# Optimization experiments

Measured on AMD Instinct MI355X. Metric: run time of the kernel, lower is better.

The kernel has to match this reference:

```python
import math
import jax, jax.numpy as jnp
import numpy as np

D_MODEL = 1024
N_HEADS = 16


def setup_inputs() -> dict:
    key = jax.random.key(0)
    ks = jax.random.split(key, 5)
    B, S, D = 4, 2048, D_MODEL
    std = math.sqrt(2.0 / (D + D))
    x = jax.random.normal(ks[0], (B, S, D), dtype=jnp.float32)
    wq = jax.random.normal(ks[1], (D, D), dtype=jnp.float32) * std
    wk = jax.random.normal(ks[2], (D, D), dtype=jnp.float32) * std
    wv = jax.random.normal(ks[3], (D, D), dtype=jnp.float32) * std
    wo = jax.random.normal(ks[4], (D, D), dtype=jnp.float32) * std
    return {"x": x, "wq": wq, "wk": wk, "wv": wv, "wo": wo}


def reference(x, wq, wk, wv, wo):
    B, S, D = x.shape
    H = N_HEADS
    dk = D // H
    # projections: weight is (d_out, d_in) -> y_...j = x_...i W_ji
    def proj(w):
        y = jnp.einsum('bsi,ji->bsj', x, w)
        return y.reshape(B, S, H, dk).transpose(0, 2, 1, 3)  # b h s dk
    Q, K, V = proj(wq), proj(wk), proj(wv)
    scores = jnp.einsum('bhnd,bhmd->bhnm', Q, K) / math.sqrt(dk)
    causal = jnp.tril(jnp.ones((S, S), dtype=bool))  # True = attend
    scores = jnp.where(causal, scores, -jnp.inf)
    weights = jax.nn.softmax(scores, axis=-1)
    attn = jnp.einsum('bhnm,bhmd->bhnd', weights, V)
    attn = attn.transpose(0, 2, 1, 3).reshape(B, S, D)
    return jnp.einsum('bsi,ji->bsj', attn, wo)
```

## Files before the change

### kernel.cpp

```cpp
#include <hip/hip_runtime.h>
#include <hip/hip_bf16.h>
#include <cstdint>

#define D_MODEL 1024
#define NHEADS  16
#define DK      64
#define BATCH   4
#define SEQ     2048
#define MROWS   (BATCH * SEQ)
#define NQT2    (SEQ / 128)
#define NW_ELEM (D_MODEL * D_MODEL)

#define QSCALE 0.18033688011112042f

typedef __attribute__((ext_vector_type(4))) float  f32x4;
typedef __attribute__((ext_vector_type(8))) __bf16 bf16x8;
typedef __attribute__((ext_vector_type(8))) short  short8;

__device__ __forceinline__ unsigned short f2bf(float f) {
    unsigned int u = __float_as_uint(f);
    unsigned int r = (u + 0x7fffu + ((u >> 16) & 1u)) >> 16;
    return (unsigned short)r;
}

__device__ __forceinline__ unsigned int cvtpk_bf16(float lo, float hi) {
    unsigned int r;
    asm volatile("v_cvt_pk_bf16_f32 %0, %1, %2" : "=v"(r) : "v"(lo), "v"(hi));
    return r;
}

__device__ __forceinline__ float exp2_raw(float x) {
    float r;
    asm("v_exp_f32 %0, %1" : "=v"(r) : "v"(x));
    return r;
}

__device__ __forceinline__ void permlane32_swap(unsigned int& a, unsigned int& b) {
    asm("v_permlane32_swap_b32 %0, %1" : "+v"(a), "+v"(b));
}
__device__ __forceinline__ void permlane16_swap(unsigned int& a, unsigned int& b) {
    asm("v_permlane16_swap_b32 %0, %1" : "+v"(a), "+v"(b));
}

__global__ void cvt_bf16(const float* __restrict__ in, unsigned short* __restrict__ out, int n) {
    int i = (blockIdx.x * 256 + threadIdx.x) * 4;
    if (i >= n) return;
    float4 v = *reinterpret_cast<const float4*>(in + i);
    ushort4 o;
    o.x = f2bf(v.x); o.y = f2bf(v.y); o.z = f2bf(v.z); o.w = f2bf(v.w);
    *reinterpret_cast<ushort4*>(out + i) = o;
}

__global__ void cvt_bf16_w(const float* __restrict__ w0, const float* __restrict__ w1,
                           const float* __restrict__ w2, const float* __restrict__ w3,
                           unsigned short* __restrict__ o0, unsigned short* __restrict__ o1,
                           unsigned short* __restrict__ o2, unsigned short* __restrict__ o3,
                           int n) {
    const int z = blockIdx.y;
    const float* in = (z == 0) ? w0 : (z == 1) ? w1 : (z == 2) ? w2 : w3;
    unsigned short* out = (z == 0) ? o0 : (z == 1) ? o1 : (z == 2) ? o2 : o3;
    int i = (blockIdx.x * 256 + threadIdx.x) * 4;
    if (i >= n) return;
    float4 v = *reinterpret_cast<const float4*>(in + i);
    ushort4 o;
    o.x = f2bf(v.x); o.y = f2bf(v.y); o.z = f2bf(v.z); o.w = f2bf(v.w);
    *reinterpret_cast<ushort4*>(out + i) = o;
}

__device__ __forceinline__ void gload_lds16(const void* g, void* l) {
    __builtin_amdgcn_global_load_lds(
        (const __attribute__((address_space(1))) void*)(uintptr_t)g,
        (__attribute__((address_space(3))) void*)(unsigned int)(uintptr_t)l,
        16, 0, 0);
}

#define BM 128
#define BN 128
#define BK 32

__global__ __launch_bounds__(256, 2) void gemm_qkv(
    const unsigned short* __restrict__ A,
    const unsigned short* __restrict__ W,
    unsigned short* __restrict__ Cq,
    unsigned short* __restrict__ Ck,
    unsigned short* __restrict__ Cv)
{
    __shared__ __align__(16) unsigned short As[2][BM * BK];
    __shared__ __align__(16) unsigned short Bs[3][2][BN * BK];

    const int K = D_MODEL, N = D_MODEL;
    const int tid  = threadIdx.x;
    const int wave = tid >> 6;
    const int lane = tid & 63;
    const int wr   = wave >> 1;
    const int wc   = wave & 1;
    const int bm   = (blockIdx.x >> 3) * BM;
    const int bn   = (blockIdx.x & 7) * BN;

    f32x4 acc[3][4][4];
    #pragma unroll
    for (int w = 0; w < 3; w++)
        #pragma unroll
        for (int i = 0; i < 4; i++)
            #pragma unroll
            for (int j = 0; j < 4; j++)
                #pragma unroll
                for (int r = 0; r < 4; r++) acc[w][i][j][r] = 0.f;

    const int srow = tid >> 2;
    const int scol = (tid & 3) * 8;

    const int kg = (lane >> 4) * 8;
    const int rl = lane & 15;

    const unsigned short* Arow0 = A + (size_t)(bm + srow) * K + scol;
    const unsigned short* Arow1 = A + (size_t)(bm + 64 + srow) * K + scol;
    const unsigned short* Wrow0 = W + (size_t)(bn + srow) * K + scol;
    const unsigned short* Wrow1 = W + (size_t)(bn + 64 + srow) * K + scol;

    auto STAGE = [&](int buf, int k0) {
        gload_lds16(Arow0 + k0, &As[buf][0] + wave * 512);
        gload_lds16(Arow1 + k0, &As[buf][0] + 2048 + wave * 512);
        #pragma unroll
        for (int w = 0; w < 3; w++) {
            gload_lds16(Wrow0 + (size_t)w * NW_ELEM + k0, &Bs[w][buf][0] + wave * 512);
            gload_lds16(Wrow1 + (size_t)w * NW_ELEM + k0, &Bs[w][buf][0] + 2048 + wave * 512);
        }
    };

    auto COMPUTE = [&](int buf) {
        bf16x8 a[4];
        #pragma unroll
        for (int mi = 0; mi < 4; mi++) {
            short8 t = *reinterpret_cast<const short8*>(&As[buf][(wr * 64 + mi * 16 + rl) * BK + kg]);
            a[mi] = __builtin_bit_cast(bf16x8, t);
        }
        #pragma unroll
        for (int w = 0; w < 3; w++)
            #pragma unroll
            for (int ni = 0; ni < 4; ni++) {
                short8 t = *reinterpret_cast<const short8*>(&Bs[w][buf][(wc * 64 + ni * 16 + rl) * BK + kg]);
                bf16x8 b = __builtin_bit_cast(bf16x8, t);
                #pragma unroll
                for (int mi = 0; mi < 4; mi++)
                    acc[w][mi][ni] = __builtin_amdgcn_mfma_f32_16x16x32_bf16(a[mi], b, acc[w][mi][ni], 0, 0, 0);
            }
    };

    const int NT = K / BK;

    STAGE(0, 0);
    __syncthreads();

    int cur = 0;
    for (int t = 0; t < NT - 1; ++t) {
        STAGE(cur ^ 1, (t + 1) * BK);
        COMPUTE(cur);
        __syncthreads();
        cur ^= 1;
    }
    COMPUTE(cur);

    const int rg = (lane >> 4) * 4;
    #pragma unroll
    for (int w = 0; w < 3; w++) {
        unsigned short* C = (w == 0) ? Cq : (w == 1) ? Ck : Cv;
        const float cs = (w == 0) ? QSCALE : 1.0f;
        #pragma unroll
        for (int mi = 0; mi < 4; mi++)
            #pragma unroll
            for (int ni = 0; ni < 4; ni++)
                #pragma unroll
                for (int r = 0; r < 4; r++) {
                    int row = bm + wr * 64 + mi * 16 + rg + r;
                    int col = bn + wc * 64 + ni * 16 + rl;
                    C[(size_t)row * N + col] = f2bf(acc[w][mi][ni][r] * cs);
                }
    }
}

__global__ __launch_bounds__(256) void gemm_out(
    const unsigned short* __restrict__ A,
    const unsigned short* __restrict__ Bt,
    float* __restrict__ C)
{
    __shared__ __align__(16) unsigned short As[2][BM * BK];
    __shared__ __align__(16) unsigned short Bs[2][BN * BK];

    const int K = D_MODEL, N = D_MODEL;
    const int tid  = threadIdx.x;
    const int wave = tid >> 6;
    const int lane = tid & 63;
    const int wr   = wave >> 1;
    const int wc   = wave & 1;
    const int bm   = (blockIdx.x >> 3) * BM;
    const int bn   = (blockIdx.x & 7) * BN;

    f32x4 acc[4][4];
    #pragma unroll
    for (int i = 0; i < 4; i++)
        #pragma unroll
        for (int j = 0; j < 4; j++)
            #pragma unroll
            for (int r = 0; r < 4; r++) acc[i][j][r] = 0.f;

    const int srow = tid >> 2;
    const int scol = (tid & 3) * 8;

    const int kg = (lane >> 4) * 8;
    const int rl = lane & 15;

    const unsigned short* Arow0 = A  + (size_t)(bm + srow) * K + scol;
    const unsigned short* Arow1 = A  + (size_t)(bm + 64 + srow) * K + scol;
    const unsigned short* Brow0 = Bt + (size_t)(bn + srow) * K + scol;
    const unsigned short* Brow1 = Bt + (size_t)(bn + 64 + srow) * K + scol;

    auto STAGE = [&](int buf, int k0) {
        gload_lds16(Arow0 + k0, &As[buf][0] + wave * 512);
        gload_lds16(Arow1 + k0, &As[buf][0] + 2048 + wave * 512);
        gload_lds16(Brow0 + k0, &Bs[buf][0] + wave * 512);
        gload_lds16(Brow1 + k0, &Bs[buf][0] + 2048 + wave * 512);
    };

    auto COMPUTE = [&](int buf) {
        bf16x8 a[4], b[4];
        #pragma unroll
        for (int mi = 0; mi < 4; mi++) {
            short8 t = *reinterpret_cast<const short8*>(&As[buf][(wr * 64 + mi * 16 + rl) * BK + kg]);
            a[mi] = __builtin_bit_cast(bf16x8, t);
        }
        #pragma unroll
        for (int ni = 0; ni < 4; ni++) {
            short8 t = *reinterpret_cast<const short8*>(&Bs[buf][(wc * 64 + ni * 16 + rl) * BK + kg]);
            b[ni] = __builtin_bit_cast(bf16x8, t);
        }
        #pragma unroll
        for (int mi = 0; mi < 4; mi++)
            #pragma unroll
            for (int ni = 0; ni < 4; ni++)
                acc[mi][ni] = __builtin_amdgcn_mfma_f32_16x16x32_bf16(a[mi], b[ni], acc[mi][ni], 0, 0, 0);
    };

    const int NT = K / BK;

    STAGE(0, 0);
    __syncthreads();

    int cur = 0;
    for (int t = 0; t < NT - 1; ++t) {
        STAGE(cur ^ 1, (t + 1) * BK);
        COMPUTE(cur);
        __syncthreads();
        cur ^= 1;
    }
    COMPUTE(cur);

    const int rg = (lane >> 4) * 4;
    #pragma unroll
    for (int mi = 0; mi < 4; mi++)
        #pragma unroll
        for (int ni = 0; ni < 4; ni++)
            #pragma unroll
            for (int r = 0; r < 4; r++) {
                int row = bm + wr * 64 + mi * 16 + rg + r;
                int col = bn + wc * 64 + ni * 16 + rl;
                C[(size_t)row * N + col] = acc[mi][ni][r];
            }
}

__global__ __launch_bounds__(512, 4) void attn_mfma(
    const unsigned short* __restrict__ Q,
    const unsigned short* __restrict__ K,
    const unsigned short* __restrict__ V,
    unsigned short* __restrict__ O)
{
    __shared__ __align__(16) unsigned short Ks[2][64 * 64];
    __shared__ __align__(16) unsigned short Vt[2][64 * 64];

    const int bh  = blockIdx.x;
    const int b   = bh >> 4;
    const int h   = bh & 15;
    const int qt  = NQT2 - 1 - blockIdx.y;
    const int tid = threadIdx.x;
    const int wave = tid >> 6;
    const int lane = tid & 63;
    const int lg   = lane >> 4;
    const int lq   = lane & 15;

    const size_t base = ((size_t)b * SEQ) * D_MODEL + h * DK;
    const unsigned short* Kb = K + base;
    const unsigned short* Vb = V + base;

    const int qw  = qt * 128 + wave * 16;
    const int myq = qw + lq;

    bf16x8 qf[2];
    {
        const unsigned short* qp = Q + base + (size_t)myq * D_MODEL + lg * 8;
        qf[0] = __builtin_bit_cast(bf16x8, *reinterpret_cast<const short8*>(qp));
        qf[1] = __builtin_bit_cast(bf16x8, *reinterpret_cast<const short8*>(qp + 32));
    }

    const short8 ones_s = {(short)0x3F80, (short)0x3F80, (short)0x3F80, (short)0x3F80,
                           (short)0x3F80, (short)0x3F80, (short)0x3F80, (short)0x3F80};
    const bf16x8 onesf = __builtin_bit_cast(bf16x8, ones_s);

    f32x4 acc[4];
    f32x4 acc_l;
    #pragma unroll
    for (int i = 0; i < 4; i++)
        #pragma unroll
        for (int r = 0; r < 4; r++) acc[i][r] = 0.f;
    #pragma unroll
    for (int r = 0; r < 4; r++) acc_l[r] = 0.f;

    const int trow  = tid >> 3;
    const int tslot = tid & 7;
    const unsigned short* Ksrc = Kb + (size_t)trow * D_MODEL + (tslot ^ (trow & 7)) * 8;

    const int vg  = tid >> 5;
    const int vd0 = (tid & 31) * 2;
    const unsigned short* Vsrc = Vb + (size_t)(4 * vg) * D_MODEL + vd0;
    unsigned int vpre[4];

    const int va0 = vd0 * 128 + ((vg * 8) ^ ((vd0 & 7) << 4));
    const int va1 = (vd0 + 1) * 128 + ((vg * 8) ^ (((vd0 + 1) & 7) << 4));

    auto VWRITE = [&](int buf) {
        unsigned int lo01 = (vpre[0] & 0xffffu) | (vpre[1] << 16);
        unsigned int lo23 = (vpre[2] & 0xffffu) | (vpre[3] << 16);
        unsigned int hi01 = (vpre[0] >> 16) | (vpre[1] & 0xffff0000u);
        unsigned int hi23 = (vpre[2] >> 16) | (vpre[3] & 0xffff0000u);
        *reinterpret_cast<uint2*>((char*)&Vt[buf][0] + va0) = make_uint2(lo01, lo23);
        *reinterpret_cast<uint2*>((char*)&Vt[buf][0] + va1) = make_uint2(hi01, hi23);
    };

    const int nt = 2 * qt + 2;

    gload_lds16(Ksrc, &Ks[0][0] + wave * 512);
    #pragma unroll
    for (int k = 0; k < 4; ++k)
        vpre[k] = *reinterpret_cast<const unsigned int*>(Vsrc + (size_t)k * D_MODEL);
    VWRITE(0);
    __syncthreads();

    for (int t = 0; t < nt; ++t) {
        const int c = t & 1;
        const bool pf = (t + 1 < nt);

        if (pf) {
            const size_t moff = (size_t)(t + 1) * 64 * D_MODEL;
            gload_lds16(Ksrc + moff, &Ks[c ^ 1][0] + wave * 512);
            #pragma unroll
            for (int k = 0; k < 4; ++k)
                vpre[k] = *reinterpret_cast<const unsigned int*>(Vsrc + moff + (size_t)k * D_MODEL);
        }

        const int m0 = t * 64;

        if (m0 <= qw + 15) {
            f32x4 s[4];
            __builtin_amdgcn_s_setprio(1);
            #pragma unroll
            for (int kg = 0; kg < 4; ++kg) {
                #pragma unroll
                for (int r = 0; r < 4; ++r) s[kg][r] = 0.f;
                #pragma unroll
                for (int ks = 0; ks < 2; ++ks) {
                    const int row  = kg * 16 + lq;
                    const int slot = (ks * 4 + lg) ^ (row & 7);
                    bf16x8 kf = __builtin_bit_cast(bf16x8,
                        *reinterpret_cast<const short8*>((const char*)&Ks[c][0] + row * 128 + slot * 16));
                    s[kg] = __builtin_amdgcn_mfma_f32_16x16x32_bf16(kf, qf[ks], s[kg], 0, 0, 0);
                }
            }
            __builtin_amdgcn_s_setprio(0);

            if (m0 + 63 > qw) {
                #pragma unroll
                for (int kg = 0; kg < 4; ++kg)
                    #pragma unroll
                    for (int r = 0; r < 4; ++r)
                        if (m0 + kg * 16 + lg * 4 + r > myq) s[kg][r] = -INFINITY;
            }

            #pragma unroll
            for (int kg = 0; kg < 4; ++kg)
                #pragma unroll
                for (int r = 0; r < 4; ++r)
                    s[kg][r] = exp2_raw(s[kg][r]);

            #pragma unroll
            for (int ks = 0; ks < 2; ++ks) {
                unsigned int A0 = cvtpk_bf16(s[2*ks][0],   s[2*ks][1]);
                unsigned int A1 = cvtpk_bf16(s[2*ks][2],   s[2*ks][3]);
                unsigned int B0 = cvtpk_bf16(s[2*ks+1][0], s[2*ks+1][1]);
                unsigned int B1 = cvtpk_bf16(s[2*ks+1][2], s[2*ks+1][3]);
                permlane32_swap(A0, B0);
                permlane16_swap(A0, B0);
                permlane32_swap(A1, B1);
                permlane16_swap(A1, B1);
                uint4 awv = make_uint4(A0, A1, B0, B1);
                bf16x8 af = __builtin_bit_cast(bf16x8, awv);
                __builtin_amdgcn_s_setprio(1);
                #pragma unroll
                for (int dg = 0; dg < 4; ++dg) {
                    const int d = dg * 16 + lq;
                    const int addr = d * 128 + ((ks * 64 + lg * 16) ^ ((d & 7) << 4));
                    bf16x8 vf = __builtin_bit_cast(bf16x8,
                        *reinterpret_cast<const short8*>((const char*)&Vt[c][0] + addr));
                    acc[dg] = __builtin_amdgcn_mfma_f32_16x16x32_bf16(af, vf, acc[dg], 0, 0, 0);
                }
                acc_l = __builtin_amdgcn_mfma_f32_16x16x32_bf16(af, onesf, acc_l, 0, 0, 0);
                __builtin_amdgcn_s_setprio(0);
            }
        }

        if (pf) VWRITE(c ^ 1);
        __syncthreads();
    }

    float lv[4];
    #pragma unroll
    for (int r = 0; r < 4; ++r) lv[r] = 1.0f / acc_l[r];
    #pragma unroll
    for (int dg = 0; dg < 4; ++dg)
        #pragma unroll
        for (int r = 0; r < 4; ++r) {
            const int qrow = qw + lg * 4 + r;
            O[base + (size_t)qrow * D_MODEL + dg * 16 + lq] = f2bf(acc[dg][r] * lv[r]);
        }
}

extern "C" void kernel_launch(void* const* d_in, const int* in_sizes, int n_in,
                              void* d_out, int out_size, void* d_ws, size_t ws_size,
                              hipStream_t stream) {
    const float* x  = (const float*)d_in[0];
    const float* wq = (const float*)d_in[1];
    const float* wk = (const float*)d_in[2];
    const float* wv = (const float*)d_in[3];
    const float* wo = (const float*)d_in[4];

    char* ws = (char*)d_ws;
    const size_t NXB = (size_t)MROWS * D_MODEL * 2;
    const size_t NWB = (size_t)D_MODEL * D_MODEL * 2;

    unsigned short* xb  = (unsigned short*)(ws);
    unsigned short* wqb = (unsigned short*)(ws + NXB);
    unsigned short* wkb = (unsigned short*)(ws + NXB + NWB);
    unsigned short* wvb = (unsigned short*)(ws + NXB + 2 * NWB);
    unsigned short* wob = (unsigned short*)(ws + NXB + 3 * NWB);
    unsigned short* Qb  = (unsigned short*)(ws + NXB + 4 * NWB);
    unsigned short* Kb  = (unsigned short*)(ws + NXB + 4 * NWB + NXB);
    unsigned short* Vb  = (unsigned short*)(ws + NXB + 4 * NWB + 2 * NXB);
    unsigned short* Ab  = (unsigned short*)(ws + NXB + 4 * NWB + 3 * NXB);

    const int NX = MROWS * D_MODEL;
    const int NW = D_MODEL * D_MODEL;

    cvt_bf16<<<NX / 1024, 256, 0, stream>>>(x, xb, NX);
    dim3 gw(NW / 1024, 4, 1);
    cvt_bf16_w<<<gw, 256, 0, stream>>>(wq, wk, wv, wo, wqb, wkb, wvb, wob, NW);

    gemm_qkv<<<512, 256, 0, stream>>>(xb, wqb, Qb, Kb, Vb);

    dim3 gattn(BATCH * NHEADS, NQT2, 1);
    attn_mfma<<<gattn, 512, 0, stream>>>(Qb, Kb, Vb, Ab);

    gemm_out<<<512, 256, 0, stream>>>(Ab, wob, (float*)d_out);
}
```

Baseline: 152.1 us.

## Process two 16-row query groups per wave to double K/V tile reuse

Enlarges the attention query tile from 128 to 256 rows per block, so each wave handles 32 query rows as two 16-row groups that share every K and V fragment read from LDS. This halves the number of K/V tile loads and LDS reads per query row and halves the grid along the query dimension. In exchange it raises register pressure (two sets of score and accumulator registers), gives coarser causal work granularity with fewer blocks, and lets more waves sit idle on masked tiles near the diagonal.

```diff
diff --git a/kernel.cpp b/kernel.cpp
--- a/kernel.cpp
+++ b/kernel.cpp
@@ -8,7 +8,7 @@
 #define BATCH   4
 #define SEQ     2048
 #define MROWS   (BATCH * SEQ)
-#define NQT2    (SEQ / 128)
+#define NQT3    (SEQ / 256)
 #define NW_ELEM (D_MODEL * D_MODEL)
 
 #define QSCALE 0.18033688011112042f
@@ -280,7 +280,7 @@
     const int bh  = blockIdx.x;
     const int b   = bh >> 4;
     const int h   = bh & 15;
-    const int qt  = NQT2 - 1 - blockIdx.y;
+    const int qt  = NQT3 - 1 - blockIdx.y;
     const int tid = threadIdx.x;
     const int wave = tid >> 6;
     const int lane = tid & 63;
@@ -291,28 +291,34 @@
     const unsigned short* Kb = K + base;
     const unsigned short* Vb = V + base;
 
-    const int qw  = qt * 128 + wave * 16;
+    const int qw  = qt * 256 + wave * 32;
     const int myq = qw + lq;
 
-    bf16x8 qf[2];
+    bf16x8 qf[2][2];
     {
-        const unsigned short* qp = Q + base + (size_t)myq * D_MODEL + lg * 8;
-        qf[0] = __builtin_bit_cast(bf16x8, *reinterpret_cast<const short8*>(qp));
-        qf[1] = __builtin_bit_cast(bf16x8, *reinterpret_cast<const short8*>(qp + 32));
+        const unsigned short* qp0 = Q + base + (size_t)myq * D_MODEL + lg * 8;
+        qf[0][0] = __builtin_bit_cast(bf16x8, *reinterpret_cast<const short8*>(qp0));
+        qf[0][1] = __builtin_bit_cast(bf16x8, *reinterpret_cast<const short8*>(qp0 + 32));
+        const unsigned short* qp1 = qp0 + 16 * D_MODEL;
+        qf[1][0] = __builtin_bit_cast(bf16x8, *reinterpret_cast<const short8*>(qp1));
+        qf[1][1] = __builtin_bit_cast(bf16x8, *reinterpret_cast<const short8*>(qp1 + 32));
     }
 
     const short8 ones_s = {(short)0x3F80, (short)0x3F80, (short)0x3F80, (short)0x3F80,
                            (short)0x3F80, (short)0x3F80, (short)0x3F80, (short)0x3F80};
     const bf16x8 onesf = __builtin_bit_cast(bf16x8, ones_s);
 
-    f32x4 acc[4];
-    f32x4 acc_l;
-    #pragma unroll
-    for (int i = 0; i < 4; i++)
-        #pragma unroll
-        for (int r = 0; r < 4; r++) acc[i][r] = 0.f;
-    #pragma unroll
-    for (int r = 0; r < 4; r++) acc_l[r] = 0.f;
+    f32x4 acc[2][4];
+    f32x4 acc_l[2];
+    #pragma unroll
+    for (int g = 0; g < 2; g++) {
+        #pragma unroll
+        for (int i = 0; i < 4; i++)
+            #pragma unroll
+            for (int r = 0; r < 4; r++) acc[g][i][r] = 0.f;
+        #pragma unroll
+        for (int r = 0; r < 4; r++) acc_l[g][r] = 0.f;
+    }
 
     const int trow  = tid >> 3;
     const int tslot = tid & 7;
@@ -335,7 +341,7 @@
         *reinterpret_cast<uint2*>((char*)&Vt[buf][0] + va1) = make_uint2(hi01, hi23);
     };
 
-    const int nt = 2 * qt + 2;
+    const int nt = 4 * qt + 4;
 
     gload_lds16(Ksrc, &Ks[0][0] + wave * 512);
     #pragma unroll
@@ -358,20 +364,21 @@
 
         const int m0 = t * 64;
 
-        if (m0 <= qw + 15) {
-            f32x4 s[4];
+        if (m0 <= qw + 31) {
+            f32x4 s0[4], s1[4];
             __builtin_amdgcn_s_setprio(1);
             #pragma unroll
             for (int kg = 0; kg < 4; ++kg) {
                 #pragma unroll
-                for (int r = 0; r < 4; ++r) s[kg][r] = 0.f;
+                for (int r = 0; r < 4; ++r) { s0[kg][r] = 0.f; s1[kg][r] = 0.f; }
                 #pragma unroll
                 for (int ks = 0; ks < 2; ++ks) {
                     const int row  = kg * 16 + lq;
                     const int slot = (ks * 4 + lg) ^ (row & 7);
                     bf16x8 kf = __builtin_bit_cast(bf16x8,
                         *reinterpret_cast<const short8*>((const char*)&Ks[c][0] + row * 128 + slot * 16));
-                    s[kg] = __builtin_amdgcn_mfma_f32_16x16x32_bf16(kf, qf[ks], s[kg], 0, 0, 0);
+                    s0[kg] = __builtin_amdgcn_mfma_f32_16x16x32_bf16(kf, qf[0][ks], s0[kg], 0, 0, 0);
+                    s1[kg] = __builtin_amdgcn_mfma_f32_16x16x32_bf16(kf, qf[1][ks], s1[kg], 0, 0, 0);
                 }
             }
             __builtin_amdgcn_s_setprio(0);
@@ -380,28 +387,43 @@
                 #pragma unroll
                 for (int kg = 0; kg < 4; ++kg)
                     #pragma unroll
-                    for (int r = 0; r < 4; ++r)
-                        if (m0 + kg * 16 + lg * 4 + r > myq) s[kg][r] = -INFINITY;
+                    for (int r = 0; r < 4; ++r) {
+                        const int key = m0 + kg * 16 + lg * 4 + r;
+                        if (key > myq)      s0[kg][r] = -INFINITY;
+                        if (key > myq + 16) s1[kg][r] = -INFINITY;
+                    }
             }
 
             #pragma unroll
             for (int kg = 0; kg < 4; ++kg)
                 #pragma unroll
-                for (int r = 0; r < 4; ++r)
-                    s[kg][r] = exp2_raw(s[kg][r]);
+                for (int r = 0; r < 4; ++r) {
+                    s0[kg][r] = exp2_raw(s0[kg][r]);
+                    s1[kg][r] = exp2_raw(s1[kg][r]);
+                }
 
             #pragma unroll
             for (int ks = 0; ks < 2; ++ks) {
-                unsigned int A0 = cvtpk_bf16(s[2*ks][0],   s[2*ks][1]);
-                unsigned int A1 = cvtpk_bf16(s[2*ks][2],   s[2*ks][3]);
-                unsigned int B0 = cvtpk_bf16(s[2*ks+1][0], s[2*ks+1][1]);
-                unsigned int B1 = cvtpk_bf16(s[2*ks+1][2], s[2*ks+1][3]);
+                unsigned int A0 = cvtpk_bf16(s0[2*ks][0],   s0[2*ks][1]);
+                unsigned int A1 = cvtpk_bf16(s0[2*ks][2],   s0[2*ks][3]);
+                unsigned int B0 = cvtpk_bf16(s0[2*ks+1][0], s0[2*ks+1][1]);
+                unsigned int B1 = cvtpk_bf16(s0[2*ks+1][2], s0[2*ks+1][3]);
                 permlane32_swap(A0, B0);
                 permlane16_swap(A0, B0);
                 permlane32_swap(A1, B1);
                 permlane16_swap(A1, B1);
-                uint4 awv = make_uint4(A0, A1, B0, B1);
-                bf16x8 af = __builtin_bit_cast(bf16x8, awv);
+                bf16x8 af0 = __builtin_bit_cast(bf16x8, make_uint4(A0, A1, B0, B1));
+
+                unsigned int C0 = cvtpk_bf16(s1[2*ks][0],   s1[2*ks][1]);
+                unsigned int C1 = cvtpk_bf16(s1[2*ks][2],   s1[2*ks][3]);
+                unsigned int D0 = cvtpk_bf16(s1[2*ks+1][0], s1[2*ks+1][1]);
+                unsigned int D1 = cvtpk_bf16(s1[2*ks+1][2], s1[2*ks+1][3]);
+                permlane32_swap(C0, D0);
+                permlane16_swap(C0, D0);
+                permlane32_swap(C1, D1);
+                permlane16_swap(C1, D1);
+                bf16x8 af1 = __builtin_bit_cast(bf16x8, make_uint4(C0, C1, D0, D1));
+
                 __builtin_amdgcn_s_setprio(1);
                 #pragma unroll
                 for (int dg = 0; dg < 4; ++dg) {
@@ -409,9 +431,11 @@
                     const int addr = d * 128 + ((ks * 64 + lg * 16) ^ ((d & 7) << 4));
                     bf16x8 vf = __builtin_bit_cast(bf16x8,
                         *reinterpret_cast<const short8*>((const char*)&Vt[c][0] + addr));
-                    acc[dg] = __builtin_amdgcn_mfma_f32_16x16x32_bf16(af, vf, acc[dg], 0, 0, 0);
+                    acc[0][dg] = __builtin_amdgcn_mfma_f32_16x16x32_bf16(af0, vf, acc[0][dg], 0, 0, 0);
+                    acc[1][dg] = __builtin_amdgcn_mfma_f32_16x16x32_bf16(af1, vf, acc[1][dg], 0, 0, 0);
                 }
-                acc_l = __builtin_amdgcn_mfma_f32_16x16x32_bf16(af, onesf, acc_l, 0, 0, 0);
+                acc_l[0] = __builtin_amdgcn_mfma_f32_16x16x32_bf16(af0, onesf, acc_l[0], 0, 0, 0);
+                acc_l[1] = __builtin_amdgcn_mfma_f32_16x16x32_bf16(af1, onesf, acc_l[1], 0, 0, 0);
                 __builtin_amdgcn_s_setprio(0);
             }
         }
@@ -420,16 +444,19 @@
         __syncthreads();
     }
 
-    float lv[4];
-    #pragma unroll
-    for (int r = 0; r < 4; ++r) lv[r] = 1.0f / acc_l[r];
-    #pragma unroll
-    for (int dg = 0; dg < 4; ++dg)
-        #pragma unroll
-        for (int r = 0; r < 4; ++r) {
-            const int qrow = qw + lg * 4 + r;
-            O[base + (size_t)qrow * D_MODEL + dg * 16 + lq] = f2bf(acc[dg][r] * lv[r]);
-        }
+    #pragma unroll
+    for (int g = 0; g < 2; ++g) {
+        float lv[4];
+        #pragma unroll
+        for (int r = 0; r < 4; ++r) lv[r] = 1.0f / acc_l[g][r];
+        #pragma unroll
+        for (int dg = 0; dg < 4; ++dg)
+            #pragma unroll
+            for (int r = 0; r < 4; ++r) {
+                const int qrow = qw + g * 16 + lg * 4 + r;
+                O[base + (size_t)qrow * D_MODEL + dg * 16 + lq] = f2bf(acc[g][dg][r] * lv[r]);
+            }
+    }
 }
 
 extern "C" void kernel_launch(void* const* d_in, const int* in_sizes, int n_in,
@@ -464,7 +491,7 @@
 
     gemm_qkv<<<512, 256, 0, stream>>>(xb, wqb, Qb, Kb, Vb);
 
-    dim3 gattn(BATCH * NHEADS, NQT2, 1);
+    dim3 gattn(BATCH * NHEADS, NQT3, 1);
     attn_mfma<<<gattn, 512, 0, stream>>>(Qb, Kb, Vb, Ab);
 
     gemm_out<<<512, 256, 0, stream>>>(Ab, wob, (float*)d_out);
```

Result: no change. 153.5 us (+0.9%).
